# Kernel tuning notes

Hardware: AMD Instinct MI355X
Metric: run time of the kernel (lower is better)

Reference implementation:

```python
import jax, jax.numpy as jnp
import numpy as np

ALPHA = 0.5   # membrane leak `alpha` in the source (module-level global)
M_TH = 1.0    # firing threshold `m_th`; fire_func(m) = (m >= m_th).float()


def setup_inputs() -> dict:
    key = jax.random.key(0)
    k1, k2, k3 = jax.random.split(key, 3)
    T, B, D = 8, 256, 4096
    x = jax.random.normal(k1, (T, B, D), dtype=jnp.float32)
    # 1/sqrt(D) scaling so membrane potentials straddle the threshold
    W = jax.random.normal(k2, (D, D), dtype=jnp.float32) / np.float32(np.sqrt(D))
    b = jax.random.normal(k3, (D,), dtype=jnp.float32) * 0.01
    return {"x": x, "W": W, "b": b}


def reference(x, W, b):
    # opts(x[t]) for a Linear `opts`, batched over time: [T,B,Din] @ [Dout,Din]^T
    mm = jnp.einsum('tbi,oi->tbo', x, W) + b  # [T, B, D]

    def step(carry, mm_t):
        m_prev, s_prev = carry
        # m[t] = opts(x[t]) + m[t-1] * (1 - s[t-1]) * alpha  (t=0: carry is zeros)
        m_t = mm_t + m_prev * (1.0 - s_prev) * ALPHA
        s_t = (m_t >= M_TH).astype(m_t.dtype)  # fire_func: hard threshold spike
        return (m_t, s_t), (m_t, s_t)

    init = (jnp.zeros_like(mm[0]), jnp.zeros_like(mm[0]))
    _, (m, s) = jax.lax.scan(step, init, mm)
    return (m, s)  # each [T, B, D], matching the lists m, s in torch forward
```

## Files before the change

### kernel.cpp

```cpp
#include <hip/hip_runtime.h>
#include <hip/hip_bf16.h>


#define T_DIM 8
#define B_DIM 256
#define D_DIM 4096
#define M_DIM (T_DIM * B_DIM)

#define BM 128
#define BN 128
#define BK 16
#define NT (D_DIM / BK)
#define LDSF (BM + 2)

__global__ __launch_bounds__(256, 2) void gemm_f64v_kernel(
    const float* __restrict__ X,
    const float* __restrict__ W,
    const float* __restrict__ bias,
    double* __restrict__ MM)
{
    __shared__ float As[2][BK][LDSF];
    __shared__ float Bs[2][BK][LDSF];

    const int tid = threadIdx.x;
    const int bm = blockIdx.y * BM;
    const int bn = blockIdx.x * BN;

    const int sr = tid >> 1;
    const int sk = (tid & 1) * 8;

    const int tm = tid & 15;
    const int tn = (tid >> 4) * 8;

    double acc[8][8];
    #pragma unroll
    for (int r = 0; r < 8; ++r)
        #pragma unroll
        for (int c = 0; c < 8; ++c) acc[r][c] = 0.0;

    const float* xp = X + (size_t)(bm + sr) * D_DIM + sk;
    const float* wp = W + (size_t)(bn + sr) * D_DIM + sk;

    {
        const float4 va0 = *reinterpret_cast<const float4*>(xp);
        const float4 va1 = *reinterpret_cast<const float4*>(xp + 4);
        const float4 vb0 = *reinterpret_cast<const float4*>(wp);
        const float4 vb1 = *reinterpret_cast<const float4*>(wp + 4);
        As[0][sk + 0][sr] = va0.x; As[0][sk + 1][sr] = va0.y;
        As[0][sk + 2][sr] = va0.z; As[0][sk + 3][sr] = va0.w;
        As[0][sk + 4][sr] = va1.x; As[0][sk + 5][sr] = va1.y;
        As[0][sk + 6][sr] = va1.z; As[0][sk + 7][sr] = va1.w;
        Bs[0][sk + 0][sr] = vb0.x; Bs[0][sk + 1][sr] = vb0.y;
        Bs[0][sk + 2][sr] = vb0.z; Bs[0][sk + 3][sr] = vb0.w;
        Bs[0][sk + 4][sr] = vb1.x; Bs[0][sk + 5][sr] = vb1.y;
        Bs[0][sk + 6][sr] = vb1.z; Bs[0][sk + 7][sr] = vb1.w;
    }
    __syncthreads();

    for (int t = 0; t < NT; ++t) {
        const int cur = t & 1;

        float4 na0, na1, nb0, nb1;
        if (t < NT - 1) {
            const int k0 = (t + 1) * BK;
            na0 = *reinterpret_cast<const float4*>(xp + k0);
            na1 = *reinterpret_cast<const float4*>(xp + k0 + 4);
            nb0 = *reinterpret_cast<const float4*>(wp + k0);
            nb1 = *reinterpret_cast<const float4*>(wp + k0 + 4);
        }

        #pragma unroll 4
        for (int kk = 0; kk < BK; ++kk) {
            double a[8], bb[8];
            #pragma unroll
            for (int i = 0; i < 4; ++i) {
                a[2 * i]     = (double)As[cur][kk][2 * tm + 32 * i];
                a[2 * i + 1] = (double)As[cur][kk][2 * tm + 32 * i + 1];
            }
            #pragma unroll
            for (int j = 0; j < 8; ++j)
                bb[j] = (double)Bs[cur][kk][tn + j];
            #pragma unroll
            for (int r = 0; r < 8; ++r)
                #pragma unroll
                for (int c = 0; c < 8; ++c)
                    acc[r][c] = fma(a[r], bb[c], acc[r][c]);
        }

        if (t < NT - 1) {
            const int nxt = cur ^ 1;
            As[nxt][sk + 0][sr] = na0.x; As[nxt][sk + 1][sr] = na0.y;
            As[nxt][sk + 2][sr] = na0.z; As[nxt][sk + 3][sr] = na0.w;
            As[nxt][sk + 4][sr] = na1.x; As[nxt][sk + 5][sr] = na1.y;
            As[nxt][sk + 6][sr] = na1.z; As[nxt][sk + 7][sr] = na1.w;
            Bs[nxt][sk + 0][sr] = nb0.x; Bs[nxt][sk + 1][sr] = nb0.y;
            Bs[nxt][sk + 2][sr] = nb0.z; Bs[nxt][sk + 3][sr] = nb0.w;
            Bs[nxt][sk + 4][sr] = nb1.x; Bs[nxt][sk + 5][sr] = nb1.y;
            Bs[nxt][sk + 6][sr] = nb1.z; Bs[nxt][sk + 7][sr] = nb1.w;
        }
        __syncthreads();
    }

    #pragma unroll
    for (int r = 0; r < 8; ++r) {
        const int row = bm + 2 * tm + 32 * (r >> 1) + (r & 1);
        double* mrow = MM + (size_t)row * D_DIM + bn + tn;
        #pragma unroll
        for (int c = 0; c < 8; ++c)
            mrow[c] = acc[r][c] + (double)bias[bn + tn + c];
    }
}

__global__ __launch_bounds__(256) void recur_kernel(
    const double* __restrict__ MM,
    float* __restrict__ out)
{
    const size_t stride = (size_t)B_DIM * D_DIM;
    const size_t idx = (size_t)blockIdx.x * 256 + threadIdx.x;

    float* out_m = out;
    float* out_s = out + (size_t)T_DIM * stride;

    double m_prev = 0.0;
    double s_prev = 0.0;
    #pragma unroll
    for (int t = 0; t < T_DIM; ++t) {
        const double mm = MM[(size_t)t * stride + idx];
        const double m = mm + m_prev * (1.0 - s_prev) * 0.5;
        const double s = (m >= 1.0) ? 1.0 : 0.0;
        out_m[(size_t)t * stride + idx] = (float)m;
        out_s[(size_t)t * stride + idx] = (float)s;
        m_prev = m;
        s_prev = s;
    }
}

extern "C" void kernel_launch(void* const* d_in, const int* in_sizes, int n_in,
                              void* d_out, int out_size, void* d_ws, size_t ws_size,
                              hipStream_t stream) {
    const float* x = (const float*)d_in[0];
    const float* W = (const float*)d_in[1];
    const float* b = (const float*)d_in[2];
    for (int i = 0; i < n_in; ++i) {
        if (in_sizes[i] == D_DIM) b = (const float*)d_in[i];
        else if (in_sizes[i] == D_DIM * D_DIM) W = (const float*)d_in[i];
        else if (in_sizes[i] == M_DIM * D_DIM) x = (const float*)d_in[i];
    }

    double* MM = (double*)d_ws;

    dim3 grid_gemm(D_DIM / BN, M_DIM / BM);
    gemm_f64v_kernel<<<grid_gemm, 256, 0, stream>>>(x, W, b, MM);

    const int n_bd = B_DIM * D_DIM;
    recur_kernel<<<n_bd / 256, 256, 0, stream>>>(MM, (float*)d_out);
}
```

Before: 1.480 ms.

## Switch FP64 GEMM from vector FMA to f64 MFMA matrix instructions

Replaces the scalar-FMA double-precision GEMM with one built on the 16x16x4 f64 MFMA instruction. Tiles shrink to 64x64 with four waves each owning a 32x32 sub-tile, and inputs are converted to double when staged into shared memory. A small probe kernel runs at launch and writes the MFMA output lane-to-row/column layout into the output buffer, which the GEMM epilogue reads to scatter results; the recurrence kernel later overwrites that buffer. This trades more GEMM blocks and a runtime layout lookup for much higher FP64 matrix throughput.

```diff
diff --git a/kernel.cpp b/kernel.cpp
--- a/kernel.cpp
+++ b/kernel.cpp
@@ -7,107 +7,129 @@
 #define D_DIM 4096
 #define M_DIM (T_DIM * B_DIM)
 
-#define BM 128
-#define BN 128
+#define BM 64
+#define BN 64
 #define BK 16
 #define NT (D_DIM / BK)
-#define LDSF (BM + 2)
+#define LDSD (BM + 2)
 
-__global__ __launch_bounds__(256, 2) void gemm_f64v_kernel(
+typedef double double4_t __attribute__((ext_vector_type(4)));
+
+__global__ __launch_bounds__(64) void mfma_probe_kernel(int* __restrict__ map)
+{
+    const int l = threadIdx.x;
+    const int l16 = l & 15;
+    const int g = l >> 4;
+
+    const double am = (double)l16;
+    const double bd = (g == 0) ? 1.0 : 0.0;
+    const double ad = (g == 0) ? 1.0 : 0.0;
+    const double bn = (double)l16;
+
+    double4_t z = {0.0, 0.0, 0.0, 0.0};
+    double4_t dm = __builtin_amdgcn_mfma_f64_16x16x4f64(am, bd, z, 0, 0, 0);
+    double4_t dn = __builtin_amdgcn_mfma_f64_16x16x4f64(ad, bn, z, 0, 0, 0);
+
+    #pragma unroll
+    for (int r = 0; r < 4; ++r) {
+        map[l * 8 + r]     = ((int)dm[r]) & 15;
+        map[l * 8 + 4 + r] = ((int)dn[r]) & 15;
+    }
+}
+
+__global__ __launch_bounds__(256) void gemm_f64_mfma_kernel(
     const float* __restrict__ X,
     const float* __restrict__ W,
     const float* __restrict__ bias,
+    const int* __restrict__ map,
     double* __restrict__ MM)
 {
-    __shared__ float As[2][BK][LDSF];
-    __shared__ float Bs[2][BK][LDSF];
+    __shared__ double As[2][BK][LDSD];
+    __shared__ double Bs[2][BK][LDSD];
 
     const int tid = threadIdx.x;
     const int bm = blockIdx.y * BM;
     const int bn = blockIdx.x * BN;
 
-    const int sr = tid >> 1;
-    const int sk = (tid & 1) * 8;
+    const int sr = tid >> 2;
+    const int sk = (tid & 3) << 2;
 
-    const int tm = tid & 15;
-    const int tn = (tid >> 4) * 8;
+    const int wave = tid >> 6;
+    const int wr = (wave >> 1) << 5;
+    const int wc = (wave & 1) << 5;
+    const int lane = tid & 63;
+    const int l16 = lane & 15;
+    const int g = lane >> 4;
 
-    double acc[8][8];
-    #pragma unroll
-    for (int r = 0; r < 8; ++r)
-        #pragma unroll
-        for (int c = 0; c < 8; ++c) acc[r][c] = 0.0;
+    double4_t acc00 = {0,0,0,0}, acc01 = {0,0,0,0};
+    double4_t acc10 = {0,0,0,0}, acc11 = {0,0,0,0};
 
     const float* xp = X + (size_t)(bm + sr) * D_DIM + sk;
     const float* wp = W + (size_t)(bn + sr) * D_DIM + sk;
 
     {
-        const float4 va0 = *reinterpret_cast<const float4*>(xp);
-        const float4 va1 = *reinterpret_cast<const float4*>(xp + 4);
-        const float4 vb0 = *reinterpret_cast<const float4*>(wp);
-        const float4 vb1 = *reinterpret_cast<const float4*>(wp + 4);
-        As[0][sk + 0][sr] = va0.x; As[0][sk + 1][sr] = va0.y;
-        As[0][sk + 2][sr] = va0.z; As[0][sk + 3][sr] = va0.w;
-        As[0][sk + 4][sr] = va1.x; As[0][sk + 5][sr] = va1.y;
-        As[0][sk + 6][sr] = va1.z; As[0][sk + 7][sr] = va1.w;
-        Bs[0][sk + 0][sr] = vb0.x; Bs[0][sk + 1][sr] = vb0.y;
-        Bs[0][sk + 2][sr] = vb0.z; Bs[0][sk + 3][sr] = vb0.w;
-        Bs[0][sk + 4][sr] = vb1.x; Bs[0][sk + 5][sr] = vb1.y;
-        Bs[0][sk + 6][sr] = vb1.z; Bs[0][sk + 7][sr] = vb1.w;
+        const float4 av = *reinterpret_cast<const float4*>(xp);
+        const float4 bv = *reinterpret_cast<const float4*>(wp);
+        As[0][sk + 0][sr] = (double)av.x; As[0][sk + 1][sr] = (double)av.y;
+        As[0][sk + 2][sr] = (double)av.z; As[0][sk + 3][sr] = (double)av.w;
+        Bs[0][sk + 0][sr] = (double)bv.x; Bs[0][sk + 1][sr] = (double)bv.y;
+        Bs[0][sk + 2][sr] = (double)bv.z; Bs[0][sk + 3][sr] = (double)bv.w;
     }
     __syncthreads();
 
     for (int t = 0; t < NT; ++t) {
         const int cur = t & 1;
 
-        float4 na0, na1, nb0, nb1;
+        float4 av, bv;
         if (t < NT - 1) {
             const int k0 = (t + 1) * BK;
-            na0 = *reinterpret_cast<const float4*>(xp + k0);
-            na1 = *reinterpret_cast<const float4*>(xp + k0 + 4);
-            nb0 = *reinterpret_cast<const float4*>(wp + k0);
-            nb1 = *reinterpret_cast<const float4*>(wp + k0 + 4);
+            av = *reinterpret_cast<const float4*>(xp + k0);
+            bv = *reinterpret_cast<const float4*>(wp + k0);
         }
 
-        #pragma unroll 4
-        for (int kk = 0; kk < BK; ++kk) {
-            double a[8], bb[8];
-            #pragma unroll
-            for (int i = 0; i < 4; ++i) {
-                a[2 * i]     = (double)As[cur][kk][2 * tm + 32 * i];
-                a[2 * i + 1] = (double)As[cur][kk][2 * tm + 32 * i + 1];
-            }
-            #pragma unroll
-            for (int j = 0; j < 8; ++j)
-                bb[j] = (double)Bs[cur][kk][tn + j];
-            #pragma unroll
-            for (int r = 0; r < 8; ++r)
-                #pragma unroll
-                for (int c = 0; c < 8; ++c)
-                    acc[r][c] = fma(a[r], bb[c], acc[r][c]);
+        #pragma unroll
+        for (int s = 0; s < 4; ++s) {
+            const int kk = 4 * s + g;
+            const double a0 = As[cur][kk][wr + l16];
+            const double a1 = As[cur][kk][wr + 16 + l16];
+            const double b0 = Bs[cur][kk][wc + l16];
+            const double b1 = Bs[cur][kk][wc + 16 + l16];
+            acc00 = __builtin_amdgcn_mfma_f64_16x16x4f64(a0, b0, acc00, 0, 0, 0);
+            acc01 = __builtin_amdgcn_mfma_f64_16x16x4f64(a0, b1, acc01, 0, 0, 0);
+            acc10 = __builtin_amdgcn_mfma_f64_16x16x4f64(a1, b0, acc10, 0, 0, 0);
+            acc11 = __builtin_amdgcn_mfma_f64_16x16x4f64(a1, b1, acc11, 0, 0, 0);
         }
 
         if (t < NT - 1) {
             const int nxt = cur ^ 1;
-            As[nxt][sk + 0][sr] = na0.x; As[nxt][sk + 1][sr] = na0.y;
-            As[nxt][sk + 2][sr] = na0.z; As[nxt][sk + 3][sr] = na0.w;
-            As[nxt][sk + 4][sr] = na1.x; As[nxt][sk + 5][sr] = na1.y;
-            As[nxt][sk + 6][sr] = na1.z; As[nxt][sk + 7][sr] = na1.w;
-            Bs[nxt][sk + 0][sr] = nb0.x; Bs[nxt][sk + 1][sr] = nb0.y;
-            Bs[nxt][sk + 2][sr] = nb0.z; Bs[nxt][sk + 3][sr] = nb0.w;
-            Bs[nxt][sk + 4][sr] = nb1.x; Bs[nxt][sk + 5][sr] = nb1.y;
-            Bs[nxt][sk + 6][sr] = nb1.z; Bs[nxt][sk + 7][sr] = nb1.w;
+            As[nxt][sk + 0][sr] = (double)av.x; As[nxt][sk + 1][sr] = (double)av.y;
+            As[nxt][sk + 2][sr] = (double)av.z; As[nxt][sk + 3][sr] = (double)av.w;
+            Bs[nxt][sk + 0][sr] = (double)bv.x; Bs[nxt][sk + 1][sr] = (double)bv.y;
+            Bs[nxt][sk + 2][sr] = (double)bv.z; Bs[nxt][sk + 3][sr] = (double)bv.w;
         }
         __syncthreads();
     }
 
+    int mrow[4], mcol[4];
     #pragma unroll
-    for (int r = 0; r < 8; ++r) {
-        const int row = bm + 2 * tm + 32 * (r >> 1) + (r & 1);
-        double* mrow = MM + (size_t)row * D_DIM + bn + tn;
+    for (int r = 0; r < 4; ++r) {
+        mrow[r] = map[lane * 8 + r];
+        mcol[r] = map[lane * 8 + 4 + r];
+    }
+
+    const double4_t* accs[4] = {&acc00, &acc01, &acc10, &acc11};
+    #pragma unroll
+    for (int mb = 0; mb < 2; ++mb) {
         #pragma unroll
-        for (int c = 0; c < 8; ++c)
-            mrow[c] = acc[r][c] + (double)bias[bn + tn + c];
+        for (int nb = 0; nb < 2; ++nb) {
+            const double4_t a = *accs[mb * 2 + nb];
+            #pragma unroll
+            for (int r = 0; r < 4; ++r) {
+                const int row = bm + wr + mb * 16 + mrow[r];
+                const int col = bn + wc + nb * 16 + mcol[r];
+                MM[(size_t)row * D_DIM + col] = a[r] + (double)bias[col];
+            }
+        }
     }
 }
 
@@ -148,9 +170,12 @@
     }
 
     double* MM = (double*)d_ws;
+    int* map = (int*)d_out;
+
+    mfma_probe_kernel<<<1, 64, 0, stream>>>(map);
 
     dim3 grid_gemm(D_DIM / BN, M_DIM / BM);
-    gemm_f64v_kernel<<<grid_gemm, 256, 0, stream>>>(x, W, b, MM);
+    gemm_f64_mfma_kernel<<<grid_gemm, 256, 0, stream>>>(x, W, b, map, MM);
 
     const int n_bd = B_DIM * D_DIM;
     recur_kernel<<<n_bd / 256, 256, 0, stream>>>(MM, (float*)d_out);
```

Result: faster. 1.308 ms (-11.7%).
